# Kernel optimization log

Hardware: AMD Instinct MI355X
Metric: run time of the kernel (lower is better)

## Reference

```python
import jax, jax.numpy as jnp
import numpy as np

B, T, C, D = 8, 4096, 1024, 128  # batch, seq_len, n_embd, attn_dim


def setup_inputs() -> dict:
    key = jax.random.key(0)
    kx, kq, kk, kv = jax.random.split(key, 4)
    scale = 0.02
    return {
        "x": jax.random.normal(kx, (B, T, C), dtype=jnp.float32),
        "Wq": jax.random.normal(kq, (C, D), dtype=jnp.float32) * scale,
        "Wk": jax.random.normal(kk, (C, D), dtype=jnp.float32) * scale,
        "Wv": jax.random.normal(kv, (C, D), dtype=jnp.float32) * scale,
    }


def reference(x, Wq, Wk, Wv):
    # single-head causal self-attention (dropout in eval mode -> identity)
    q = jnp.einsum("btc,cd->btd", x, Wq)
    k = jnp.einsum("btc,cd->btd", x, Wk)
    v = jnp.einsum("btc,cd->btd", x, Wv)
    dk = q.shape[-1]
    scores = jnp.einsum("btd,bsd->bts", q, k) / jnp.sqrt(jnp.float32(dk))  # [B,T,T]
    tq = q.shape[1]
    causal = jnp.tril(jnp.ones((tq, tq), dtype=bool))
    scores = jnp.where(causal[None, :, :], scores, jnp.float32(-jnp.inf))
    weights = jax.nn.softmax(scores, axis=-1)
    return jnp.einsum("bts,bsd->btd", weights, v)
```

## Files before the change

### kernel.cpp

```cpp
#include <hip/hip_runtime.h>
#include <hip/hip_bf16.h>
#include <stdint.h>


typedef __attribute__((ext_vector_type(8))) short short8;
typedef __attribute__((ext_vector_type(4))) float f32x4;
typedef __attribute__((ext_vector_type(4))) unsigned short u16x4;

#define NB 8
#define NT 4096
#define NC 1024
#define ND 128

__device__ __forceinline__ unsigned short f2bf(float f) {
    union { float f; uint32_t u; } v; v.f = f;
    uint32_t u = v.u;
    return (unsigned short)((u + 0x7FFFu + ((u >> 16) & 1u)) >> 16);
}
__device__ __forceinline__ unsigned int pack2(float lo, float hi) {
    return ((unsigned int)f2bf(hi) << 16) | (unsigned int)f2bf(lo);
}

__global__ void prep_w(const float* __restrict__ Wq, const float* __restrict__ Wk,
                       const float* __restrict__ Wv, unsigned short* __restrict__ Wbt) {
    int idx = blockIdx.x * 256 + threadIdx.x;
    int w = idx >> 17;
    int rem = idx & 131071;
    int n = rem >> 10;
    int k = rem & 1023;
    const float* W = (w == 0) ? Wq : (w == 1) ? Wk : Wv;
    Wbt[idx] = f2bf(W[k * ND + n]);
}

__global__ __launch_bounds__(256, 3)
void qkv_gemm(const float* __restrict__ x, const unsigned short* __restrict__ Wbt,
              unsigned short* __restrict__ Qo, unsigned short* __restrict__ Ko,
              unsigned short* __restrict__ Vto) {
    __shared__ __align__(16) float Al[128 * 64];
    __shared__ __align__(16) unsigned short Bl[128 * 64];
    const int mt = blockIdx.x, nt = blockIdx.y;
    const int tid = threadIdx.x;
    const int lane = tid & 63;
    const int w = tid >> 6;
    const int wr = w >> 1, wc = w & 1;
    const int l15 = lane & 15, lg = lane >> 4;
    const int m0 = mt * 128;
    const unsigned short* Wn = Wbt + (size_t)nt * (ND * NC);

    f32x4 acc[4][4];
#pragma unroll
    for (int i = 0; i < 4; ++i)
#pragma unroll
        for (int j = 0; j < 4; ++j) acc[i][j] = (f32x4)0.0f;

    for (int ks = 0; ks < 16; ++ks) {
        const int k0 = ks * 64;
#pragma unroll
        for (int r = 0; r < 8; ++r) {
            int o = r * 4096 + tid * 16;
            int row = o >> 8;
            int colb = (o & 255) ^ ((row & 7) << 4);
            const float* src = x + (size_t)(m0 + row) * NC + k0 + (colb >> 2);
            __builtin_amdgcn_global_load_lds(
                (const __attribute__((address_space(1))) void*)src,
                (__attribute__((address_space(3))) void*)((char*)Al + o), 16, 0, 0);
        }
#pragma unroll
        for (int r = 0; r < 4; ++r) {
            int o = r * 4096 + tid * 16;
            int row = o >> 7;
            int colb = (o & 127) ^ ((row & 7) << 4);
            const unsigned short* src = Wn + (size_t)row * NC + k0 + (colb >> 1);
            __builtin_amdgcn_global_load_lds(
                (const __attribute__((address_space(1))) void*)src,
                (__attribute__((address_space(3))) void*)((char*)Bl + o), 16, 0, 0);
        }
        __syncthreads();

#pragma unroll
        for (int kc = 0; kc < 2; ++kc) {
            short8 a[4], b[4];
#pragma unroll
            for (int mi = 0; mi < 4; ++mi) {
                const int row = wr * 64 + mi * 16 + l15;
                const int cb = (row & 7) << 4;
                const int base = row * 256;
                f32x4 lo = *reinterpret_cast<const f32x4*>(
                    (const char*)Al + base + ((kc * 128 + lg * 32) ^ cb));
                f32x4 hi = *reinterpret_cast<const f32x4*>(
                    (const char*)Al + base + ((kc * 128 + lg * 32 + 16) ^ cb));
                short8 av;
#pragma unroll
                for (int e = 0; e < 4; ++e) {
                    av[e] = (short)f2bf(lo[e]);
                    av[4 + e] = (short)f2bf(hi[e]);
                }
                a[mi] = av;
            }
#pragma unroll
            for (int ni = 0; ni < 4; ++ni) {
                const int row = wc * 64 + ni * 16 + l15;
                const int cb = (row & 7) << 4;
                b[ni] = *reinterpret_cast<const short8*>(
                    (const char*)Bl + row * 128 + ((kc * 64 + lg * 16) ^ cb));
            }
#pragma unroll
            for (int mi = 0; mi < 4; ++mi)
#pragma unroll
                for (int ni = 0; ni < 4; ++ni)
                    acc[mi][ni] = __builtin_amdgcn_mfma_f32_16x16x32_bf16(
                        a[mi], b[ni], acc[mi][ni], 0, 0, 0);
        }
        __syncthreads();
    }
#pragma unroll
    for (int mi = 0; mi < 4; ++mi)
#pragma unroll
        for (int ni = 0; ni < 4; ++ni)
#pragma unroll
            for (int r = 0; r < 4; ++r) {
                int row = m0 + wr * 64 + mi * 16 + lg * 4 + r;
                int col = wc * 64 + ni * 16 + l15;
                unsigned short bv = f2bf(acc[mi][ni][r]);
                if (nt == 0) Qo[(size_t)row * ND + col] = bv;
                else if (nt == 1) Ko[(size_t)row * ND + col] = bv;
                else {
                    int bb2 = row >> 12, t = row & 4095;
                    Vto[((size_t)(bb2 * ND + col)) * NT + t] = bv;
                }
            }
}

__global__ __launch_bounds__(512, 2)
void attn_fwd(const unsigned short* __restrict__ Q, const unsigned short* __restrict__ K,
              const unsigned short* __restrict__ Vt, float* __restrict__ out) {
    __shared__ __align__(16) char smem[149504];

    const int bid = blockIdx.x;
    const int p = bid >> 3, b = bid & 7;
    const int tid = threadIdx.x;
    const int w = tid >> 6, lane = tid & 63;
    const int l15 = lane & 15, lg = lane >> 4;
    const int g = w >> 2, wq = w & 3;

    const float sc = 0.08838834764831845f;
    const float L2E = 1.4426950408889634f;

    unsigned short* Kg = (unsigned short*)(smem + g * 32768);
    unsigned short* Vg = (unsigned short*)(smem + 65536 + g * 32768);
    unsigned short* pw = (unsigned short*)(smem + 131072 + w * 2304);
    float* mOp = (float*)(smem) + wq * 2048;
    float* mml = (float*)(smem + 32768) + wq * 32;

    const unsigned short* Kbase = &K[(size_t)b * NT * ND];
    const unsigned short* Vbase = &Vt[(size_t)b * ND * NT];

    auto stage = [&](int buf, int s0) {
#pragma unroll
        for (int r = 0; r < 4; ++r) {
            int off = r * 4096 + wq * 1024 + lane * 16;
            int row = off >> 8;
            int gcol = (off & 255) ^ ((row & 7) << 4);
            const unsigned short* src = Kbase + (size_t)(s0 + row) * ND + (gcol >> 1);
            __builtin_amdgcn_global_load_lds(
                (const __attribute__((address_space(1))) void*)src,
                (__attribute__((address_space(3))) void*)(Kg + ((buf * 16384 + r * 4096 + wq * 1024) >> 1)),
                16, 0, 0);
        }
#pragma unroll
        for (int r = 0; r < 4; ++r) {
            int off = r * 4096 + wq * 1024 + lane * 16;
            int row = off >> 7;
            int gcol = (off & 127) ^ ((row & 7) << 4);
            const unsigned short* src = Vbase + (size_t)row * NT + s0 + (gcol >> 1);
            __builtin_amdgcn_global_load_lds(
                (const __attribute__((address_space(1))) void*)src,
                (__attribute__((address_space(3))) void*)(Vg + ((buf * 16384 + r * 4096 + wq * 1024) >> 1)),
                16, 0, 0);
        }
    };

    for (int half = 0; half < 2; ++half) {
        const int qt = half ? (63 - p) : p;
        const int qb0 = qt * 64;
        const int qw0 = qb0 + wq * 16;
        const int niter = (qt + 2) >> 1;

        short8 qf[4];
        const size_t qbase = ((size_t)b * NT + qw0 + l15) * ND;
#pragma unroll
        for (int c = 0; c < 4; ++c)
            qf[c] = *reinterpret_cast<const short8*>(&Q[qbase + c * 32 + lg * 8]);

        f32x4 o[8];
#pragma unroll
        for (int jn = 0; jn < 8; ++jn) o[jn] = (f32x4)0.0f;
        float mrow = -1e30f, lsum = 0.0f;

        if (g <= qt) stage(0, g * 64);
        __syncthreads();
        int cur = 0;

        for (int i = 0; i < niter; ++i) {
            const int t = 2 * i + g;
            const int s0 = t * 64;
            if (t + 2 <= qt) stage(cur ^ 1, (t + 2) * 64);

            if (t <= qt) {
                const unsigned short* KlC = Kg + cur * 8192;
                f32x4 s[4];
#pragma unroll
                for (int j = 0; j < 4; ++j) s[j] = (f32x4)0.0f;
                __builtin_amdgcn_s_setprio(1);
#pragma unroll
                for (int j = 0; j < 4; ++j) {
                    const int row = j * 16 + l15;
                    const int cb = (row & 7) << 4;
#pragma unroll
                    for (int c = 0; c < 4; ++c) {
                        short8 kf = *reinterpret_cast<const short8*>(
                            &KlC[row * 128 + (((c * 64 + lg * 16) ^ cb) >> 1)]);
                        s[j] = __builtin_amdgcn_mfma_f32_16x16x32_bf16(kf, qf[c], s[j], 0, 0, 0);
                    }
                }
                __builtin_amdgcn_s_setprio(0);

                const unsigned short* VlC = Vg + cur * 8192;
                short8 vf0[8];
#pragma unroll
                for (int jn = 0; jn < 4; ++jn) {
                    const int row = jn * 16 + l15;
                    const int cb = (row & 7) << 4;
#pragma unroll
                    for (int kc = 0; kc < 2; ++kc)
                        vf0[jn * 2 + kc] = *reinterpret_cast<const short8*>(
                            &VlC[row * 64 + (((kc * 64 + lg * 16) ^ cb) >> 1)]);
                }

                const bool diag = (s0 + 64 > qw0);
                float pmax = -1e30f;
#pragma unroll
                for (int j = 0; j < 4; ++j)
#pragma unroll
                    for (int r = 0; r < 4; ++r) {
                        float sv = s[j][r] * sc;
                        if (diag && (s0 + j * 16 + lg * 4 + r > qw0 + l15)) sv = -1e30f;
                        s[j][r] = sv;
                        pmax = fmaxf(pmax, sv);
                    }
                pmax = fmaxf(pmax, __shfl_xor(pmax, 16, 64));
                pmax = fmaxf(pmax, __shfl_xor(pmax, 32, 64));
                float mn = fmaxf(mrow, pmax);
                float alpha = exp2f((mrow - mn) * L2E);
                mrow = mn;
                float psum = 0.0f;
#pragma unroll
                for (int j = 0; j < 4; ++j)
#pragma unroll
                    for (int r = 0; r < 4; ++r) {
                        float pv = exp2f((s[j][r] - mn) * L2E);
                        s[j][r] = pv;
                        psum += pv;
                    }
                psum += __shfl_xor(psum, 16, 64);
                psum += __shfl_xor(psum, 32, 64);
                lsum = lsum * alpha + psum;

#pragma unroll
                for (int j = 0; j < 4; ++j) {
                    uint2 val;
                    val.x = pack2(s[j][0], s[j][1]);
                    val.y = pack2(s[j][2], s[j][3]);
                    *reinterpret_cast<uint2*>(&pw[l15 * 72 + j * 16 + lg * 4]) = val;
                }
                asm volatile("s_waitcnt lgkmcnt(0)" ::: "memory");
                short8 pa[2];
#pragma unroll
                for (int kc = 0; kc < 2; ++kc)
                    pa[kc] = *reinterpret_cast<const short8*>(&pw[l15 * 72 + kc * 32 + lg * 8]);

                float aT[4];
#pragma unroll
                for (int r = 0; r < 4; ++r) aT[r] = __shfl(alpha, lg * 4 + r, 64);
#pragma unroll
                for (int jn = 0; jn < 8; ++jn)
#pragma unroll
                    for (int r = 0; r < 4; ++r) o[jn][r] *= aT[r];

                __builtin_amdgcn_s_setprio(1);
#pragma unroll
                for (int jn = 0; jn < 4; ++jn)
#pragma unroll
                    for (int kc = 0; kc < 2; ++kc)
                        o[jn] = __builtin_amdgcn_mfma_f32_16x16x32_bf16(
                            pa[kc], vf0[jn * 2 + kc], o[jn], 0, 0, 0);
#pragma unroll
                for (int jn = 4; jn < 8; ++jn) {
                    const int row = jn * 16 + l15;
                    const int cb = (row & 7) << 4;
#pragma unroll
                    for (int kc = 0; kc < 2; ++kc) {
                        short8 vf = *reinterpret_cast<const short8*>(
                            &VlC[row * 64 + (((kc * 64 + lg * 16) ^ cb) >> 1)]);
                        o[jn] = __builtin_amdgcn_mfma_f32_16x16x32_bf16(pa[kc], vf, o[jn], 0, 0, 0);
                    }
                }
                __builtin_amdgcn_s_setprio(0);
            }

            __syncthreads();
            cur ^= 1;
        }

        if (g == 1) {
#pragma unroll
            for (int jn = 0; jn < 8; ++jn)
#pragma unroll
                for (int r = 0; r < 4; ++r)
                    mOp[(lg * 4 + r) * 128 + jn * 16 + l15] = o[jn][r];
            if (lg == 0) {
                mml[l15] = mrow;
                mml[16 + l15] = lsum;
            }
        }
        __syncthreads();
        if (g == 0) {
            float e0[4], e1[4], rL[4];
#pragma unroll
            for (int r = 0; r < 4; ++r) {
                int rr = lg * 4 + r;
                float m0T = __shfl(mrow, rr, 64);
                float l0T = __shfl(lsum, rr, 64);
                float m1 = mml[rr], l1 = mml[16 + rr];
                float M = fmaxf(m0T, m1);
                e0[r] = exp2f((m0T - M) * L2E);
                e1[r] = exp2f((m1 - M) * L2E);
                rL[r] = 1.0f / (l0T * e0[r] + l1 * e1[r]);
            }
#pragma unroll
            for (int jn = 0; jn < 8; ++jn)
#pragma unroll
                for (int r = 0; r < 4; ++r) {
                    int rr = lg * 4 + r, cc = jn * 16 + l15;
                    float v = o[jn][r] * e0[r] + mOp[rr * 128 + cc] * e1[r];
                    out[((size_t)b * NT + qw0 + rr) * ND + cc] = v * rL[r];
                }
        }
        __syncthreads();
    }
}

extern "C" void kernel_launch(void* const* d_in, const int* in_sizes, int n_in,
                              void* d_out, int out_size, void* d_ws, size_t ws_size,
                              hipStream_t stream) {
    const float* x  = (const float*)d_in[0];
    const float* Wq = (const float*)d_in[1];
    const float* Wk = (const float*)d_in[2];
    const float* Wv = (const float*)d_in[3];
    float* out = (float*)d_out;

    unsigned short* ws  = (unsigned short*)d_ws;
    unsigned short* Wbt = ws;
    unsigned short* Qb  = Wbt + 3 * ND * NC;
    unsigned short* Kb  = Qb + (size_t)NB * NT * ND;
    unsigned short* Vtb = Kb + (size_t)NB * NT * ND;

    prep_w<<<1536, 256, 0, stream>>>(Wq, Wk, Wv, Wbt);
    qkv_gemm<<<dim3(256, 3), 256, 0, stream>>>(x, Wbt, Qb, Kb, Vtb);
    attn_fwd<<<256, 512, 0, stream>>>(Qb, Kb, Vtb, out);
}
```

Baseline: 139.3 us.

## Double query rows per warp, fold softmax scale into Q, lazy rescale

Each warp now processes two 16-row query slices against each staged K/V tile, so the block covers 128 query rows and each K/V fragment read from LDS feeds twice as many MFMAs. The attention scale is folded into the Q projection epilogue, removing a multiply per score. The online-softmax max is updated only when the new block max exceeds the running max by more than a threshold, and the output rescale is skipped when no lane needs it. This doubles accumulator register use and may lower occupancy, and the grid pairing changes to 32 chunks with coarser causal load balancing.

```diff
diff --git a/kernel.cpp b/kernel.cpp
--- a/kernel.cpp
+++ b/kernel.cpp
@@ -121,7 +121,9 @@
             for (int r = 0; r < 4; ++r) {
                 int row = m0 + wr * 64 + mi * 16 + lg * 4 + r;
                 int col = wc * 64 + ni * 16 + l15;
-                unsigned short bv = f2bf(acc[mi][ni][r]);
+                float v = acc[mi][ni][r];
+                if (nt == 0) v *= 0.08838834764831845f;
+                unsigned short bv = f2bf(v);
                 if (nt == 0) Qo[(size_t)row * ND + col] = bv;
                 else if (nt == 1) Ko[(size_t)row * ND + col] = bv;
                 else {
@@ -143,14 +145,13 @@
     const int l15 = lane & 15, lg = lane >> 4;
     const int g = w >> 2, wq = w & 3;
 
-    const float sc = 0.08838834764831845f;
     const float L2E = 1.4426950408889634f;
 
     unsigned short* Kg = (unsigned short*)(smem + g * 32768);
     unsigned short* Vg = (unsigned short*)(smem + 65536 + g * 32768);
     unsigned short* pw = (unsigned short*)(smem + 131072 + w * 2304);
-    float* mOp = (float*)(smem) + wq * 2048;
-    float* mml = (float*)(smem + 32768) + wq * 32;
+    float* mO = (float*)(smem) + wq * 4096;
+    float* ml = (float*)(smem + 65536) + wq * 64;
 
     const unsigned short* Kbase = &K[(size_t)b * NT * ND];
     const unsigned short* Vbase = &Vt[(size_t)b * ND * NT];
@@ -181,128 +182,144 @@
     };
 
     for (int half = 0; half < 2; ++half) {
-        const int qt = half ? (63 - p) : p;
-        const int qb0 = qt * 64;
-        const int qw0 = qb0 + wq * 16;
-        const int niter = (qt + 2) >> 1;
-
-        short8 qf[4];
-        const size_t qbase = ((size_t)b * NT + qw0 + l15) * ND;
-#pragma unroll
-        for (int c = 0; c < 4; ++c)
-            qf[c] = *reinterpret_cast<const short8*>(&Q[qbase + c * 32 + lg * 8]);
-
-        f32x4 o[8];
-#pragma unroll
-        for (int jn = 0; jn < 8; ++jn) o[jn] = (f32x4)0.0f;
-        float mrow = -1e30f, lsum = 0.0f;
-
-        if (g <= qt) stage(0, g * 64);
+        const int c = half ? (31 - p) : p;
+        const int qw0 = c * 128 + wq * 32;
+        const int qwA = qw0, qwB = qw0 + 16;
+
+        short8 qfA[4], qfB[4];
+        const size_t qbA = ((size_t)b * NT + qwA + l15) * ND;
+        const size_t qbB = ((size_t)b * NT + qwB + l15) * ND;
+#pragma unroll
+        for (int cc = 0; cc < 4; ++cc) {
+            qfA[cc] = *reinterpret_cast<const short8*>(&Q[qbA + cc * 32 + lg * 8]);
+            qfB[cc] = *reinterpret_cast<const short8*>(&Q[qbB + cc * 32 + lg * 8]);
+        }
+
+        f32x4 oA[8], oB[8];
+#pragma unroll
+        for (int jn = 0; jn < 8; ++jn) { oA[jn] = (f32x4)0.0f; oB[jn] = (f32x4)0.0f; }
+        float mrA = -1e30f, lsA = 0.0f, mrB = -1e30f, lsB = 0.0f;
+
+        stage(0, g * 64);
         __syncthreads();
         int cur = 0;
 
-        for (int i = 0; i < niter; ++i) {
+        for (int i = 0; i <= c; ++i) {
             const int t = 2 * i + g;
             const int s0 = t * 64;
-            if (t + 2 <= qt) stage(cur ^ 1, (t + 2) * 64);
-
-            if (t <= qt) {
+            if (i < c) stage(cur ^ 1, s0 + 128);
+
+            if (s0 <= qwB) {
                 const unsigned short* KlC = Kg + cur * 8192;
-                f32x4 s[4];
-#pragma unroll
-                for (int j = 0; j < 4; ++j) s[j] = (f32x4)0.0f;
+                const unsigned short* VlC = Vg + cur * 8192;
+                const bool doA = (s0 <= qwA);
+
+                f32x4 sA[4], sB[4];
+#pragma unroll
+                for (int j = 0; j < 4; ++j) { sA[j] = (f32x4)0.0f; sB[j] = (f32x4)0.0f; }
                 __builtin_amdgcn_s_setprio(1);
 #pragma unroll
                 for (int j = 0; j < 4; ++j) {
                     const int row = j * 16 + l15;
                     const int cb = (row & 7) << 4;
 #pragma unroll
-                    for (int c = 0; c < 4; ++c) {
+                    for (int cc = 0; cc < 4; ++cc) {
                         short8 kf = *reinterpret_cast<const short8*>(
-                            &KlC[row * 128 + (((c * 64 + lg * 16) ^ cb) >> 1)]);
-                        s[j] = __builtin_amdgcn_mfma_f32_16x16x32_bf16(kf, qf[c], s[j], 0, 0, 0);
+                            &KlC[row * 128 + (((cc * 64 + lg * 16) ^ cb) >> 1)]);
+                        sA[j] = __builtin_amdgcn_mfma_f32_16x16x32_bf16(kf, qfA[cc], sA[j], 0, 0, 0);
+                        sB[j] = __builtin_amdgcn_mfma_f32_16x16x32_bf16(kf, qfB[cc], sB[j], 0, 0, 0);
                     }
                 }
                 __builtin_amdgcn_s_setprio(0);
 
-                const unsigned short* VlC = Vg + cur * 8192;
-                short8 vf0[8];
-#pragma unroll
-                for (int jn = 0; jn < 4; ++jn) {
-                    const int row = jn * 16 + l15;
-                    const int cb = (row & 7) << 4;
+                auto softmax_set = [&](f32x4 (&s)[4], float& mr, float& ls,
+                                       float& alpha, bool& need, int qrb) {
+                    const bool diag = (s0 + 64 > qrb);
+                    float pmax = -1e30f;
+#pragma unroll
+                    for (int j = 0; j < 4; ++j)
+#pragma unroll
+                        for (int r = 0; r < 4; ++r) {
+                            float sv = s[j][r];
+                            if (diag && (s0 + j * 16 + lg * 4 + r > qrb + l15)) sv = -1e30f;
+                            s[j][r] = sv;
+                            pmax = fmaxf(pmax, sv);
+                        }
+                    pmax = fmaxf(pmax, __shfl_xor(pmax, 16, 64));
+                    pmax = fmaxf(pmax, __shfl_xor(pmax, 32, 64));
+                    float mn;
+                    need = (pmax > mr + 8.0f);
+                    if (need) { mn = pmax; alpha = exp2f((mr - mn) * L2E); mr = mn; }
+                    else { mn = mr; alpha = 1.0f; }
+                    float ps = 0.0f;
+#pragma unroll
+                    for (int j = 0; j < 4; ++j)
+#pragma unroll
+                        for (int r = 0; r < 4; ++r) {
+                            float pv = exp2f((s[j][r] - mn) * L2E);
+                            s[j][r] = pv;
+                            ps += pv;
+                        }
+                    ps += __shfl_xor(ps, 16, 64);
+                    ps += __shfl_xor(ps, 32, 64);
+                    ls = ls * alpha + ps;
+                };
+                auto pack_read = [&](f32x4 (&s)[4], short8 (&pa)[2]) {
+#pragma unroll
+                    for (int j = 0; j < 4; ++j) {
+                        uint2 val;
+                        val.x = pack2(s[j][0], s[j][1]);
+                        val.y = pack2(s[j][2], s[j][3]);
+                        *reinterpret_cast<uint2*>(&pw[l15 * 72 + j * 16 + lg * 4]) = val;
+                    }
+                    asm volatile("s_waitcnt lgkmcnt(0)" ::: "memory");
 #pragma unroll
                     for (int kc = 0; kc < 2; ++kc)
-                        vf0[jn * 2 + kc] = *reinterpret_cast<const short8*>(
-                            &VlC[row * 64 + (((kc * 64 + lg * 16) ^ cb) >> 1)]);
-                }
-
-                const bool diag = (s0 + 64 > qw0);
-                float pmax = -1e30f;
-#pragma unroll
-                for (int j = 0; j < 4; ++j)
+                        pa[kc] = *reinterpret_cast<const short8*>(
+                            &pw[l15 * 72 + kc * 32 + lg * 8]);
+                    asm volatile("s_waitcnt lgkmcnt(0)" ::: "memory");
+                };
+
+                float alphaA = 1.0f, alphaB = 1.0f;
+                bool needA = false, needB = false;
+                short8 paA[2], paB[2];
+                if (doA) {
+                    softmax_set(sA, mrA, lsA, alphaA, needA, qwA);
+                    pack_read(sA, paA);
+                }
+                softmax_set(sB, mrB, lsB, alphaB, needB, qwB);
+                pack_read(sB, paB);
+
+                if (__any((int)(needA || needB))) {
+                    float aTA[4], aTB[4];
 #pragma unroll
                     for (int r = 0; r < 4; ++r) {
-                        float sv = s[j][r] * sc;
-                        if (diag && (s0 + j * 16 + lg * 4 + r > qw0 + l15)) sv = -1e30f;
-                        s[j][r] = sv;
-                        pmax = fmaxf(pmax, sv);
+                        aTA[r] = __shfl(alphaA, lg * 4 + r, 64);
+                        aTB[r] = __shfl(alphaB, lg * 4 + r, 64);
                     }
-                pmax = fmaxf(pmax, __shfl_xor(pmax, 16, 64));
-                pmax = fmaxf(pmax, __shfl_xor(pmax, 32, 64));
-                float mn = fmaxf(mrow, pmax);
-                float alpha = exp2f((mrow - mn) * L2E);
-                mrow = mn;
-                float psum = 0.0f;
-#pragma unroll
-                for (int j = 0; j < 4; ++j)
-#pragma unroll
-                    for (int r = 0; r < 4; ++r) {
-                        float pv = exp2f((s[j][r] - mn) * L2E);
-                        s[j][r] = pv;
-                        psum += pv;
-                    }
-                psum += __shfl_xor(psum, 16, 64);
-                psum += __shfl_xor(psum, 32, 64);
-                lsum = lsum * alpha + psum;
-
-#pragma unroll
-                for (int j = 0; j < 4; ++j) {
-                    uint2 val;
-                    val.x = pack2(s[j][0], s[j][1]);
-                    val.y = pack2(s[j][2], s[j][3]);
-                    *reinterpret_cast<uint2*>(&pw[l15 * 72 + j * 16 + lg * 4]) = val;
-                }
-                asm volatile("s_waitcnt lgkmcnt(0)" ::: "memory");
-                short8 pa[2];
-#pragma unroll
-                for (int kc = 0; kc < 2; ++kc)
-                    pa[kc] = *reinterpret_cast<const short8*>(&pw[l15 * 72 + kc * 32 + lg * 8]);
-
-                float aT[4];
-#pragma unroll
-                for (int r = 0; r < 4; ++r) aT[r] = __shfl(alpha, lg * 4 + r, 64);
-#pragma unroll
-                for (int jn = 0; jn < 8; ++jn)
-#pragma unroll
-                    for (int r = 0; r < 4; ++r) o[jn][r] *= aT[r];
+#pragma unroll
+                    for (int jn = 0; jn < 8; ++jn)
+#pragma unroll
+                        for (int r = 0; r < 4; ++r) {
+                            oA[jn][r] *= aTA[r];
+                            oB[jn][r] *= aTB[r];
+                        }
+                }
 
                 __builtin_amdgcn_s_setprio(1);
 #pragma unroll
-                for (int jn = 0; jn < 4; ++jn)
-#pragma unroll
-                    for (int kc = 0; kc < 2; ++kc)
-                        o[jn] = __builtin_amdgcn_mfma_f32_16x16x32_bf16(
-                            pa[kc], vf0[jn * 2 + kc], o[jn], 0, 0, 0);
-#pragma unroll
-                for (int jn = 4; jn < 8; ++jn) {
+                for (int jn = 0; jn < 8; ++jn) {
                     const int row = jn * 16 + l15;
                     const int cb = (row & 7) << 4;
 #pragma unroll
                     for (int kc = 0; kc < 2; ++kc) {
                         short8 vf = *reinterpret_cast<const short8*>(
                             &VlC[row * 64 + (((kc * 64 + lg * 16) ^ cb) >> 1)]);
-                        o[jn] = __builtin_amdgcn_mfma_f32_16x16x32_bf16(pa[kc], vf, o[jn], 0, 0, 0);
+                        if (doA)
+                            oA[jn] = __builtin_amdgcn_mfma_f32_16x16x32_bf16(
+                                paA[kc], vf, oA[jn], 0, 0, 0);
+                        oB[jn] = __builtin_amdgcn_mfma_f32_16x16x32_bf16(
+                            paB[kc], vf, oB[jn], 0, 0, 0);
                     }
                 }
                 __builtin_amdgcn_s_setprio(0);
@@ -316,34 +333,49 @@
 #pragma unroll
             for (int jn = 0; jn < 8; ++jn)
 #pragma unroll
-                for (int r = 0; r < 4; ++r)
-                    mOp[(lg * 4 + r) * 128 + jn * 16 + l15] = o[jn][r];
+                for (int r = 0; r < 4; ++r) {
+                    mO[(lg * 4 + r) * 128 + jn * 16 + l15] = oA[jn][r];
+                    mO[(16 + lg * 4 + r) * 128 + jn * 16 + l15] = oB[jn][r];
+                }
             if (lg == 0) {
-                mml[l15] = mrow;
-                mml[16 + l15] = lsum;
+                ml[0 * 16 + l15] = mrA;
+                ml[1 * 16 + l15] = lsA;
+                ml[2 * 16 + l15] = mrB;
+                ml[3 * 16 + l15] = lsB;
             }
         }
         __syncthreads();
         if (g == 0) {
-            float e0[4], e1[4], rL[4];
+            float e0A[4], e1A[4], rLA[4], e0B[4], e1B[4], rLB[4];
 #pragma unroll
             for (int r = 0; r < 4; ++r) {
                 int rr = lg * 4 + r;
-                float m0T = __shfl(mrow, rr, 64);
-                float l0T = __shfl(lsum, rr, 64);
-                float m1 = mml[rr], l1 = mml[16 + rr];
-                float M = fmaxf(m0T, m1);
-                e0[r] = exp2f((m0T - M) * L2E);
-                e1[r] = exp2f((m1 - M) * L2E);
-                rL[r] = 1.0f / (l0T * e0[r] + l1 * e1[r]);
+                {
+                    float m0T = __shfl(mrA, rr, 64), l0T = __shfl(lsA, rr, 64);
+                    float m1 = ml[0 * 16 + rr], l1 = ml[1 * 16 + rr];
+                    float M = fmaxf(m0T, m1);
+                    e0A[r] = exp2f((m0T - M) * L2E);
+                    e1A[r] = exp2f((m1 - M) * L2E);
+                    rLA[r] = 1.0f / (l0T * e0A[r] + l1 * e1A[r]);
+                }
+                {
+                    float m0T = __shfl(mrB, rr, 64), l0T = __shfl(lsB, rr, 64);
+                    float m1 = ml[2 * 16 + rr], l1 = ml[3 * 16 + rr];
+                    float M = fmaxf(m0T, m1);
+                    e0B[r] = exp2f((m0T - M) * L2E);
+                    e1B[r] = exp2f((m1 - M) * L2E);
+                    rLB[r] = 1.0f / (l0T * e0B[r] + l1 * e1B[r]);
+                }
             }
 #pragma unroll
             for (int jn = 0; jn < 8; ++jn)
 #pragma unroll
                 for (int r = 0; r < 4; ++r) {
                     int rr = lg * 4 + r, cc = jn * 16 + l15;
-                    float v = o[jn][r] * e0[r] + mOp[rr * 128 + cc] * e1[r];
-                    out[((size_t)b * NT + qw0 + rr) * ND + cc] = v * rL[r];
+                    float vA = oA[jn][r] * e0A[r] + mO[rr * 128 + cc] * e1A[r];
+                    out[((size_t)b * NT + qwA + rr) * ND + cc] = vA * rLA[r];
+                    float vB = oB[jn][r] * e0B[r] + mO[(16 + rr) * 128 + cc] * e1B[r];
+                    out[((size_t)b * NT + qwB + rr) * ND + cc] = vB * rLB[r];
                 }
         }
         __syncthreads();
```

New measurement: 195.6 us. 40.4% more time.
